# Kernel optimization log

Hardware: AMD Instinct MI355X
Metric: run time of the kernel (lower is better)

Reference implementation:

```python
import jax, jax.numpy as jnp
import numpy as np

B, S, D, H = 2, 2048, 1024, 16
HD = D // H  # head_dim = 64
SCALE = HD ** -0.5


def setup_inputs() -> dict:
    key = jax.random.key(0)
    k1, k2, k3 = jax.random.split(key, 3)
    src = jax.random.normal(k1, (B, S, D), dtype=jnp.float32)
    w_qkv = jax.random.normal(k2, (D, 3 * D), dtype=jnp.float32) * (D ** -0.5)
    b_qkv = jax.random.normal(k3, (3 * D,), dtype=jnp.float32) * 0.02
    return {"src": src, "w_qkv": w_qkv, "b_qkv": b_qkv}


def reference(src, w_qkv, b_qkv):
    # qkv projection: [B,S,3D]
    qkv = src @ w_qkv + b_qkv
    q, k, v = jnp.split(qkv, 3, axis=-1)
    # [B,S,D] -> [B,H,S,HD]
    def heads(x):
        return x.reshape(B, S, H, HD).transpose(0, 2, 1, 3)
    q, k, v = heads(q), heads(k), heads(v)
    # scaled dot-product attention (note: original scales AFTER q@k.T)
    attn = jnp.einsum('bhqd,bhkd->bhqk', q, k) * SCALE
    attn = jax.nn.softmax(attn, axis=-1)
    out = jnp.einsum('bhqk,bhkd->bhqd', attn, v)  # [B,H,S,HD]
    return out.transpose(0, 2, 1, 3).reshape(B, S, D)
```

## Files before the change

kernel.cpp:

```cpp
#include <hip/hip_runtime.h>
#include <hip/hip_bf16.h>

typedef short short8 __attribute__((ext_vector_type(8)));
typedef float f32x4 __attribute__((ext_vector_type(4)));
typedef float f32x16 __attribute__((ext_vector_type(16)));
typedef __hip_bfloat16 bf16;


__device__ __forceinline__ void glds16(const void* g, void* l) {
  __builtin_amdgcn_global_load_lds((const __attribute__((address_space(1))) unsigned int*)g,
                                   (__attribute__((address_space(3))) unsigned int*)l, 16, 0, 0);
}

__device__ __forceinline__ uint pk2(float a, float b) {
  union { bf16 h2[2]; uint u; } pk;
  pk.h2[0] = __float2bfloat16(a);
  pk.h2[1] = __float2bfloat16(b);
  return pk.u;
}

__global__ __launch_bounds__(256) void cvt_src_kernel(const float4* __restrict__ in,
                                                      bf16* __restrict__ out, int n4) {
  int i = blockIdx.x * 256 + threadIdx.x;
  if (i >= n4) return;
  float4 v = in[i];
  union { bf16 h[4]; uint2 u; } pk;
  pk.h[0] = __float2bfloat16(v.x);
  pk.h[1] = __float2bfloat16(v.y);
  pk.h[2] = __float2bfloat16(v.z);
  pk.h[3] = __float2bfloat16(v.w);
  *(uint2*)(out + (size_t)i * 4) = pk.u;
}

__global__ __launch_bounds__(256) void transpose_w_kernel(const float* __restrict__ w,
                                                          bf16* __restrict__ wt) {
  __shared__ float tile[32][33];
  int x0 = blockIdx.x * 32;
  int y0 = blockIdx.y * 32;
  int tx = threadIdx.x & 31, ty = threadIdx.x >> 5;
#pragma unroll
  for (int i = 0; i < 4; i++) {
    int y = ty + i * 8;
    tile[y][tx] = w[(size_t)(y0 + y) * 3072 + x0 + tx];
  }
  __syncthreads();
#pragma unroll
  for (int i = 0; i < 4; i++) {
    int y = ty + i * 8;
    wt[(size_t)(x0 + y) * 1024 + y0 + tx] = __float2bfloat16(tile[tx][y]);
  }
}

__global__ __launch_bounds__(256) void qkv_gemm_kernel(
    const bf16* __restrict__ A, const bf16* __restrict__ Bt,
    const float* __restrict__ bias,
    bf16* __restrict__ q_ws, bf16* __restrict__ k_ws, bf16* __restrict__ vt_ws) {
  __shared__ alignas(16) char AB[32768];
  const int tid = threadIdx.x;
  const int lane = tid & 63, wid = tid >> 6;
  const int lr = lane & 15, lg = lane >> 4;
  const int wm = wid >> 1, wn = wid & 1;
  const int m0 = blockIdx.x * 128, n0 = blockIdx.y * 128;

  const f32x4 z4 = {0.f, 0.f, 0.f, 0.f};
  f32x4 acc[4][4];
#pragma unroll
  for (int m = 0; m < 4; m++)
#pragma unroll
    for (int n = 0; n < 4; n++) acc[m][n] = z4;

  const int srow = lane >> 3;
  const int sseg = (lane & 7) ^ srow;
  const char* Ag = (const char*)A + (size_t)(m0 + wid * 32 + srow) * 2048 + sseg * 16;
  const char* Bg = (const char*)Bt + (size_t)(n0 + wid * 32 + srow) * 2048 + sseg * 16;
  char* Al = AB + wid * 4096;
  char* Bl = AB + 16384 + wid * 4096;
  const int xora = (lr & 7) << 4;

  for (int kt = 0; kt < 16; kt++) {
    __syncthreads();
#pragma unroll
    for (int c = 0; c < 4; c++) {
      glds16(Ag + (size_t)kt * 128 + c * 16384, Al + c * 1024);
      glds16(Bg + (size_t)kt * 128 + c * 16384, Bl + c * 1024);
    }
    asm volatile("s_waitcnt vmcnt(0)" ::: "memory");
    __syncthreads();
#pragma unroll
    for (int g = 0; g < 2; g++) {
      short8 af[4], bfr[4];
#pragma unroll
      for (int m = 0; m < 4; m++)
        af[m] = *(const short8*)(AB + (wm * 64 + m * 16 + lr) * 128 +
                                 ((g * 64 + lg * 16) ^ xora));
#pragma unroll
      for (int n = 0; n < 4; n++)
        bfr[n] = *(const short8*)(AB + 16384 + (wn * 64 + n * 16 + lr) * 128 +
                                  ((g * 64 + lg * 16) ^ xora));
#pragma unroll
      for (int m = 0; m < 4; m++)
#pragma unroll
        for (int n = 0; n < 4; n++)
          acc[m][n] = __builtin_amdgcn_mfma_f32_16x16x32_bf16(af[m], bfr[n], acc[m][n], 0, 0, 0);
    }
  }

  const int which = n0 >> 10;
#pragma unroll
  for (int m = 0; m < 4; m++) {
    int row = m0 + wm * 64 + m * 16 + lg * 4;
    int b = row >> 11;
    int ss0 = row & 2047;
#pragma unroll
    for (int n = 0; n < 4; n++) {
      int col = n0 + wn * 64 + n * 16 + lr;
      int d = col & 1023;
      int h = d >> 6, hd = d & 63;
      size_t bh = (size_t)(b * 16 + h);
      float bv = bias[col];
      if (which == 2) {
        union { bf16 h4[4]; uint2 u; } pk;
#pragma unroll
        for (int r = 0; r < 4; r++) pk.h4[r] = __float2bfloat16(acc[m][n][r] + bv);
        *(uint2*)&vt_ws[(bh * 64 + hd) * 2048 + ss0] = pk.u;
      } else {
        bf16* dst = (which == 0) ? q_ws : k_ws;
#pragma unroll
        for (int r = 0; r < 4; r++)
          dst[(bh * 2048 + (ss0 + r)) * 64 + hd] = __float2bfloat16(acc[m][n][r] + bv);
      }
    }
  }
}

__global__ __launch_bounds__(512) void attn3_kernel(
    const bf16* __restrict__ q_ws, const bf16* __restrict__ k_ws,
    const bf16* __restrict__ vt_ws, float* __restrict__ out) {
  __shared__ alignas(16) char smem[65536];
  const int tid = threadIdx.x;
  const int lane = tid & 63, wid = tid >> 6;
  const int lq = lane & 31, hi = lane >> 5;
  const int hi16 = hi * 16;
  const int xorv = (lq & 7) << 4;
  const float scale_l2e = 0.125f * 1.44269504088896f;

  const int f = blockIdx.x;
  const int bh = (f & 7) * 4 + ((f >> 3) & 3);
  const int qb = f >> 5;
  const int b = bh >> 4, h = bh & 15;
  const int q0 = qb * 256 + wid * 32;

  short8 qf[4];
  {
    const bf16* qrow = q_ws + ((size_t)bh * 2048 + q0 + lq) * 64;
#pragma unroll
    for (int s = 0; s < 4; s++) qf[s] = *(const short8*)(qrow + s * 16 + hi * 8);
  }

  const int l8 = lane >> 3;
  const int segk = (lane & 7) ^ l8;
  const char* kgl = (const char*)k_ws + (size_t)bh * 262144 +
                    (size_t)(wid * 16 + l8) * 128 + segk * 16;
  const int l16 = lane >> 4;
  const int d0v = (wid * 2 + 0) * 4 + l16;
  const int d1v = (wid * 2 + 1) * 4 + l16;
  const char* vg0 = (const char*)vt_ws + (size_t)bh * 262144 + (size_t)d0v * 4096 +
                    (((lane & 15) ^ (d0v & 15)) << 4);
  const char* vg1 = (const char*)vt_ws + (size_t)bh * 262144 + (size_t)d1v * 4096 +
                    (((lane & 15) ^ (d1v & 15)) << 4);

  f32x16 o0a, o0b, o1a, o1b;
#pragma unroll
  for (int r = 0; r < 16; r++) { o0a[r] = 0.f; o0b[r] = 0.f; o1a[r] = 0.f; o1b[r] = 0.f; }
  float m = -1e30f, l = 0.f;

  glds16(kgl, smem + wid * 2048);
  glds16(kgl + 1024, smem + wid * 2048 + 1024);
  glds16(vg0, smem + 32768 + wid * 2048);
  glds16(vg1, smem + 32768 + wid * 2048 + 1024);
  asm volatile("s_waitcnt vmcnt(0)" ::: "memory");
  __builtin_amdgcn_s_barrier();

  for (int kt = 0; kt < 16; ++kt) {
    const int kb_off = (kt & 1) * 16384;
    const int vb_off = 32768 + (kt & 1) * 16384;
    if (kt + 1 < 16) {
      const int nb = ((kt + 1) & 1) * 16384;
      glds16(kgl + (size_t)(kt + 1) * 16384, smem + nb + wid * 2048);
      glds16(kgl + (size_t)(kt + 1) * 16384 + 1024, smem + nb + wid * 2048 + 1024);
      glds16(vg0 + (size_t)(kt + 1) * 256, smem + 32768 + nb + wid * 2048);
      glds16(vg1 + (size_t)(kt + 1) * 256, smem + 32768 + nb + wid * 2048 + 1024);
    }

    f32x16 s0, s1, s2, s3;
#pragma unroll
    for (int r = 0; r < 16; r++) { s0[r] = 0.f; s1[r] = 0.f; s2[r] = 0.f; s3[r] = 0.f; }
#pragma unroll
    for (int st = 0; st < 4; st++) {
      const int doff = (st * 32 + hi16) ^ xorv;
      short8 ka = *(const short8*)(smem + kb_off + lq * 128 + doff);
      short8 kb = *(const short8*)(smem + kb_off + (lq + 32) * 128 + doff);
      short8 kc = *(const short8*)(smem + kb_off + (lq + 64) * 128 + doff);
      short8 kd = *(const short8*)(smem + kb_off + (lq + 96) * 128 + doff);
      __builtin_amdgcn_s_setprio(1);
      s0 = __builtin_amdgcn_mfma_f32_32x32x16_bf16(ka, qf[st], s0, 0, 0, 0);
      s1 = __builtin_amdgcn_mfma_f32_32x32x16_bf16(kb, qf[st], s1, 0, 0, 0);
      s2 = __builtin_amdgcn_mfma_f32_32x32x16_bf16(kc, qf[st], s2, 0, 0, 0);
      s3 = __builtin_amdgcn_mfma_f32_32x32x16_bf16(kd, qf[st], s3, 0, 0, 0);
      __builtin_amdgcn_s_setprio(0);
    }

    float mx[16];
#pragma unroll
    for (int i = 0; i < 16; i++)
      mx[i] = fmaxf(fmaxf(s0[i], s1[i]), fmaxf(s2[i], s3[i]));
#pragma unroll
    for (int i = 0; i < 8; i++) mx[i] = fmaxf(mx[i], mx[i + 8]);
#pragma unroll
    for (int i = 0; i < 4; i++) mx[i] = fmaxf(mx[i], mx[i + 4]);
    float pm = fmaxf(fmaxf(mx[0], mx[1]), fmaxf(mx[2], mx[3]));
    pm = fmaxf(pm, __shfl_xor(pm, 32));
    pm *= scale_l2e;
    if (pm > m + 8.f) {
      float rs = __builtin_amdgcn_exp2f(m - pm);
      m = pm; l *= rs;
#pragma unroll
      for (int r = 0; r < 16; r++) {
        o0a[r] *= rs; o0b[r] *= rs; o1a[r] *= rs; o1b[r] *= rs;
      }
    }
#pragma unroll
    for (int r = 0; r < 16; r++) {
      s0[r] = __builtin_amdgcn_exp2f(__builtin_fmaf(s0[r], scale_l2e, -m));
      s1[r] = __builtin_amdgcn_exp2f(__builtin_fmaf(s1[r], scale_l2e, -m));
      s2[r] = __builtin_amdgcn_exp2f(__builtin_fmaf(s2[r], scale_l2e, -m));
      s3[r] = __builtin_amdgcn_exp2f(__builtin_fmaf(s3[r], scale_l2e, -m));
    }
    {
      float sm[16];
#pragma unroll
      for (int i = 0; i < 16; i++) sm[i] = (s0[i] + s1[i]) + (s2[i] + s3[i]);
#pragma unroll
      for (int i = 0; i < 8; i++) sm[i] += sm[i + 8];
#pragma unroll
      for (int i = 0; i < 4; i++) sm[i] += sm[i + 4];
      float ps = (sm[0] + sm[1]) + (sm[2] + sm[3]);
      ps += __shfl_xor(ps, 32);
      l += ps;
    }

#define PV_KB(S, KB, OA, OB)                                                     \
  {                                                                              \
    uint w0 = pk2(S[0], S[1]), w1 = pk2(S[2], S[3]);                             \
    uint w2 = pk2(S[4], S[5]), w3 = pk2(S[6], S[7]);                             \
    uint w4 = pk2(S[8], S[9]), w5 = pk2(S[10], S[11]);                           \
    uint w6 = pk2(S[12], S[13]), w7 = pk2(S[14], S[15]);                         \
    uint r0 = (uint)__shfl_xor((int)(hi ? w0 : w2), 32);                         \
    uint r1 = (uint)__shfl_xor((int)(hi ? w1 : w3), 32);                         \
    uint r2 = (uint)__shfl_xor((int)(hi ? w4 : w6), 32);                         \
    uint r3 = (uint)__shfl_xor((int)(hi ? w5 : w7), 32);                         \
    union { uint u[4]; short8 s8; } ua, ub;                                      \
    ua.u[0] = hi ? r0 : w0; ua.u[1] = hi ? r1 : w1;                              \
    ua.u[2] = hi ? w2 : r0; ua.u[3] = hi ? w3 : r1;                              \
    ub.u[0] = hi ? r2 : w4; ub.u[1] = hi ? r3 : w5;                              \
    ub.u[2] = hi ? w6 : r2; ub.u[3] = hi ? w7 : r3;                              \
    const int c0 = (((KB) * 4 + hi) ^ (lq & 15)) << 4;                           \
    const int c1 = (((KB) * 4 + 2 + hi) ^ (lq & 15)) << 4;                       \
    short8 va0 = *(const short8*)(smem + vb_off + lq * 256 + c0);                \
    short8 va1 = *(const short8*)(smem + vb_off + (lq + 32) * 256 + c0);         \
    short8 vb0 = *(const short8*)(smem + vb_off + lq * 256 + c1);                \
    short8 vb1 = *(const short8*)(smem + vb_off + (lq + 32) * 256 + c1);         \
    __builtin_amdgcn_s_setprio(1);                                               \
    OA = __builtin_amdgcn_mfma_f32_32x32x16_bf16(va0, ua.s8, OA, 0, 0, 0);       \
    OB = __builtin_amdgcn_mfma_f32_32x32x16_bf16(va1, ua.s8, OB, 0, 0, 0);       \
    OA = __builtin_amdgcn_mfma_f32_32x32x16_bf16(vb0, ub.s8, OA, 0, 0, 0);       \
    OB = __builtin_amdgcn_mfma_f32_32x32x16_bf16(vb1, ub.s8, OB, 0, 0, 0);       \
    __builtin_amdgcn_s_setprio(0);                                               \
  }
    PV_KB(s0, 0, o0a, o1a)
    PV_KB(s1, 1, o0b, o1b)
    PV_KB(s2, 2, o0a, o1a)
    PV_KB(s3, 3, o0b, o1b)
#undef PV_KB

    if (kt < 15) {
      asm volatile("s_waitcnt vmcnt(0)" ::: "memory");
      __builtin_amdgcn_s_barrier();
    }
  }
  __syncthreads();

  f32x16 o0, o1;
#pragma unroll
  for (int r = 0; r < 16; r++) { o0[r] = o0a[r] + o0b[r]; o1[r] = o1a[r] + o1b[r]; }
  float* ep = (float*)(smem) + wid * 1024;
  const float invl = 1.f / l;
  const int eq = lane >> 1, eds = lane & 1;
  float* obase = out + ((size_t)b * 2048 + qb * 256 + wid * 32 + eq) * 1024 +
                 h * 64 + eds * 16;
#pragma unroll
  for (int db = 0; db < 2; db++) {
#pragma unroll
    for (int r = 0; r < 16; r++) {
      int d = (r & 3) + 8 * (r >> 2) + 4 * hi;
      float v = (db ? o1[r] : o0[r]) * invl;
      ep[lq * 32 + ((d + lq) & 31)] = v;
    }
#pragma unroll
    for (int c = 0; c < 4; c++) {
      float4 t;
      t.x = ep[eq * 32 + ((eds * 16 + 4 * c + 0 + eq) & 31)];
      t.y = ep[eq * 32 + ((eds * 16 + 4 * c + 1 + eq) & 31)];
      t.z = ep[eq * 32 + ((eds * 16 + 4 * c + 2 + eq) & 31)];
      t.w = ep[eq * 32 + ((eds * 16 + 4 * c + 3 + eq) & 31)];
      *(float4*)(obase + db * 32 + 4 * c) = t;
    }
  }
}

extern "C" void kernel_launch(void* const* d_in, const int* in_sizes, int n_in,
                              void* d_out, int out_size, void* d_ws, size_t ws_size,
                              hipStream_t stream) {
  (void)in_sizes; (void)n_in; (void)out_size; (void)ws_size;
  const float* src  = (const float*)d_in[0];
  const float* w    = (const float*)d_in[1];
  const float* bias = (const float*)d_in[2];
  float* out = (float*)d_out;

  char* ws = (char*)d_ws;
  bf16* src_bf = (bf16*)ws;
  bf16* wt_bf  = (bf16*)(ws + 8388608);
  bf16* q_ws   = (bf16*)(ws + 8388608 + 6291456);
  bf16* k_ws   = q_ws + 4194304;
  bf16* vt_ws  = k_ws + 4194304;

  cvt_src_kernel<<<4096, 256, 0, stream>>>((const float4*)src, src_bf, 1048576);
  transpose_w_kernel<<<dim3(96, 32), 256, 0, stream>>>(w, wt_bf);
  qkv_gemm_kernel<<<dim3(32, 24), 256, 0, stream>>>(src_bf, wt_bf, bias, q_ws, k_ws, vt_ws);
  attn3_kernel<<<256, 512, 0, stream>>>(q_ws, k_ws, vt_ws, out);
}
```

Baseline: 102.7 us.

## Software-pipeline attention QK^T of next tile with softmax/PV of current; merge prep kernels

The attention kernel is restructured so the QK^T MFMAs for tile T+1 are interleaved with exp and PV work for tile T, using ping-pong score registers. K is prefetched two tiles ahead with partial vmcnt waits. The split o0a/o0b accumulators are collapsed into two, and launch bounds ask for 2 waves per SIMD. Separately, the src conversion and weight transpose kernels are merged into one launch to cut launch overhead. This adds register pressure and more barriers per iteration.

```diff
diff --git a/kernel.cpp b/kernel.cpp
--- a/kernel.cpp
+++ b/kernel.cpp
@@ -19,35 +19,37 @@
   return pk.u;
 }
 
-__global__ __launch_bounds__(256) void cvt_src_kernel(const float4* __restrict__ in,
-                                                      bf16* __restrict__ out, int n4) {
-  int i = blockIdx.x * 256 + threadIdx.x;
-  if (i >= n4) return;
-  float4 v = in[i];
-  union { bf16 h[4]; uint2 u; } pk;
-  pk.h[0] = __float2bfloat16(v.x);
-  pk.h[1] = __float2bfloat16(v.y);
-  pk.h[2] = __float2bfloat16(v.z);
-  pk.h[3] = __float2bfloat16(v.w);
-  *(uint2*)(out + (size_t)i * 4) = pk.u;
-}
-
-__global__ __launch_bounds__(256) void transpose_w_kernel(const float* __restrict__ w,
-                                                          bf16* __restrict__ wt) {
+__global__ __launch_bounds__(256) void prep_kernel(const float4* __restrict__ in,
+                                                   bf16* __restrict__ src_bf,
+                                                   const float* __restrict__ w,
+                                                   bf16* __restrict__ wt) {
   __shared__ float tile[32][33];
-  int x0 = blockIdx.x * 32;
-  int y0 = blockIdx.y * 32;
-  int tx = threadIdx.x & 31, ty = threadIdx.x >> 5;
-#pragma unroll
-  for (int i = 0; i < 4; i++) {
-    int y = ty + i * 8;
-    tile[y][tx] = w[(size_t)(y0 + y) * 3072 + x0 + tx];
-  }
-  __syncthreads();
-#pragma unroll
-  for (int i = 0; i < 4; i++) {
-    int y = ty + i * 8;
-    wt[(size_t)(x0 + y) * 1024 + y0 + tx] = __float2bfloat16(tile[tx][y]);
+  const int bid = blockIdx.x;
+  if (bid < 4096) {
+    int i = bid * 256 + threadIdx.x;
+    float4 v = in[i];
+    union { bf16 h[4]; uint2 u; } pk;
+    pk.h[0] = __float2bfloat16(v.x);
+    pk.h[1] = __float2bfloat16(v.y);
+    pk.h[2] = __float2bfloat16(v.z);
+    pk.h[3] = __float2bfloat16(v.w);
+    *(uint2*)(src_bf + (size_t)i * 4) = pk.u;
+  } else {
+    int id = bid - 4096;
+    int x0 = (id % 96) * 32;
+    int y0 = (id / 96) * 32;
+    int tx = threadIdx.x & 31, ty = threadIdx.x >> 5;
+#pragma unroll
+    for (int i = 0; i < 4; i++) {
+      int y = ty + i * 8;
+      tile[y][tx] = w[(size_t)(y0 + y) * 3072 + x0 + tx];
+    }
+    __syncthreads();
+#pragma unroll
+    for (int i = 0; i < 4; i++) {
+      int y = ty + i * 8;
+      wt[(size_t)(x0 + y) * 1024 + y0 + tx] = __float2bfloat16(tile[tx][y]);
+    }
   }
 }
 
@@ -133,7 +135,121 @@
   }
 }
 
-__global__ __launch_bounds__(512) void attn3_kernel(
+#define PV_KB(S, KB)                                                           \
+  {                                                                            \
+    uint w0 = pk2(S[0], S[1]), w1 = pk2(S[2], S[3]);                           \
+    uint w2 = pk2(S[4], S[5]), w3 = pk2(S[6], S[7]);                           \
+    uint w4 = pk2(S[8], S[9]), w5 = pk2(S[10], S[11]);                         \
+    uint w6 = pk2(S[12], S[13]), w7 = pk2(S[14], S[15]);                       \
+    uint r0 = (uint)__shfl_xor((int)(hi ? w0 : w2), 32);                       \
+    uint r1 = (uint)__shfl_xor((int)(hi ? w1 : w3), 32);                       \
+    uint r2 = (uint)__shfl_xor((int)(hi ? w4 : w6), 32);                       \
+    uint r3 = (uint)__shfl_xor((int)(hi ? w5 : w7), 32);                       \
+    union { uint u[4]; short8 s8; } ua, ub;                                    \
+    ua.u[0] = hi ? r0 : w0; ua.u[1] = hi ? r1 : w1;                            \
+    ua.u[2] = hi ? w2 : r0; ua.u[3] = hi ? w3 : r1;                            \
+    ub.u[0] = hi ? r2 : w4; ub.u[1] = hi ? r3 : w5;                            \
+    ub.u[2] = hi ? w6 : r2; ub.u[3] = hi ? w7 : r3;                            \
+    const int c0 = (((KB) * 4 + hi) ^ (lq & 15)) << 4;                         \
+    const int c1 = (((KB) * 4 + 2 + hi) ^ (lq & 15)) << 4;                     \
+    short8 va0 = *(const short8*)(smem + vbc + lq * 256 + c0);                 \
+    short8 va1 = *(const short8*)(smem + vbc + (lq + 32) * 256 + c0);          \
+    short8 vb0 = *(const short8*)(smem + vbc + lq * 256 + c1);                 \
+    short8 vb1 = *(const short8*)(smem + vbc + (lq + 32) * 256 + c1);          \
+    __builtin_amdgcn_s_setprio(1);                                             \
+    o0 = __builtin_amdgcn_mfma_f32_32x32x16_bf16(va0, ua.s8, o0, 0, 0, 0);     \
+    o1 = __builtin_amdgcn_mfma_f32_32x32x16_bf16(va1, ua.s8, o1, 0, 0, 0);     \
+    o0 = __builtin_amdgcn_mfma_f32_32x32x16_bf16(vb0, ub.s8, o0, 0, 0, 0);     \
+    o1 = __builtin_amdgcn_mfma_f32_32x32x16_bf16(vb1, ub.s8, o1, 0, 0, 0);     \
+    __builtin_amdgcn_s_setprio(0);                                             \
+  }
+
+#define QK_ST(ST, AR, B0, B1, B2, B3, QKF, KBN)                                \
+  {                                                                            \
+    if (QKF) {                                                                 \
+      const int doff = ((ST) * 32 + hi16) ^ xorv;                              \
+      short8 ka = *(const short8*)(smem + (KBN) + lq * 128 + doff);            \
+      short8 kb = *(const short8*)(smem + (KBN) + (lq + 32) * 128 + doff);     \
+      short8 kc = *(const short8*)(smem + (KBN) + (lq + 64) * 128 + doff);     \
+      short8 kd = *(const short8*)(smem + (KBN) + (lq + 96) * 128 + doff);     \
+      __builtin_amdgcn_s_setprio(1);                                           \
+      B0 = __builtin_amdgcn_mfma_f32_32x32x16_bf16(ka, qf[ST], B0, 0, 0, 0);   \
+      B1 = __builtin_amdgcn_mfma_f32_32x32x16_bf16(kb, qf[ST], B1, 0, 0, 0);   \
+      B2 = __builtin_amdgcn_mfma_f32_32x32x16_bf16(kc, qf[ST], B2, 0, 0, 0);   \
+      B3 = __builtin_amdgcn_mfma_f32_32x32x16_bf16(kd, qf[ST], B3, 0, 0, 0);   \
+      __builtin_amdgcn_s_setprio(0);                                           \
+    }                                                                          \
+    _Pragma("unroll")                                                          \
+    for (int r_ = 0; r_ < 16; r_++)                                            \
+      AR[r_] = __builtin_amdgcn_exp2f(__builtin_fmaf(AR[r_], scale_l2e, -m));  \
+  }
+
+#define ATTN_ITER(T, A0, A1, A2, A3, B0, B1, B2, B3, VMC, KF, VF, QKF, EB)     \
+  {                                                                            \
+    if (KF) {                                                                  \
+      glds16(kgl + (size_t)((T) + 2) * 16384,                                  \
+             smem + ((T) & 1) * 16384 + wid * 2048);                           \
+      glds16(kgl + (size_t)((T) + 2) * 16384 + 1024,                           \
+             smem + ((T) & 1) * 16384 + wid * 2048 + 1024);                    \
+    }                                                                          \
+    if (VF) {                                                                  \
+      glds16(vg0 + (size_t)((T) + 1) * 256,                                    \
+             smem + 32768 + (((T) + 1) & 1) * 16384 + wid * 2048);             \
+      glds16(vg1 + (size_t)((T) + 1) * 256,                                    \
+             smem + 32768 + (((T) + 1) & 1) * 16384 + wid * 2048 + 1024);      \
+    }                                                                          \
+    asm volatile("s_waitcnt vmcnt(" #VMC ")" ::: "memory");                    \
+    __builtin_amdgcn_s_barrier();                                              \
+    const int kbn = (((T) + 1) & 1) * 16384;                                   \
+    const int vbc = 32768 + ((T) & 1) * 16384;                                 \
+    if (QKF) {                                                                 \
+      _Pragma("unroll") for (int r_ = 0; r_ < 16; r_++) {                      \
+        B0[r_] = 0.f; B1[r_] = 0.f; B2[r_] = 0.f; B3[r_] = 0.f;                \
+      }                                                                        \
+    }                                                                          \
+    QK_ST(0, A0, B0, B1, B2, B3, QKF, kbn)                                     \
+    QK_ST(1, A1, B0, B1, B2, B3, QKF, kbn)                                     \
+    QK_ST(2, A2, B0, B1, B2, B3, QKF, kbn)                                     \
+    QK_ST(3, A3, B0, B1, B2, B3, QKF, kbn)                                     \
+    {                                                                          \
+      float sm_[16];                                                           \
+      _Pragma("unroll") for (int i = 0; i < 16; i++)                           \
+        sm_[i] = (A0[i] + A1[i]) + (A2[i] + A3[i]);                            \
+      _Pragma("unroll") for (int i = 0; i < 8; i++) sm_[i] += sm_[i + 8];      \
+      _Pragma("unroll") for (int i = 0; i < 4; i++) sm_[i] += sm_[i + 4];      \
+      float ps = (sm_[0] + sm_[1]) + (sm_[2] + sm_[3]);                        \
+      ps += __shfl_xor(ps, 32);                                                \
+      l += ps;                                                                 \
+    }                                                                          \
+    PV_KB(A0, 0)                                                               \
+    PV_KB(A1, 1)                                                               \
+    PV_KB(A2, 2)                                                               \
+    PV_KB(A3, 3)                                                               \
+    if (QKF) {                                                                 \
+      float mx_[16];                                                           \
+      _Pragma("unroll") for (int i = 0; i < 16; i++)                           \
+        mx_[i] = fmaxf(fmaxf(B0[i], B1[i]), fmaxf(B2[i], B3[i]));              \
+      _Pragma("unroll") for (int i = 0; i < 8; i++)                            \
+        mx_[i] = fmaxf(mx_[i], mx_[i + 8]);                                    \
+      _Pragma("unroll") for (int i = 0; i < 4; i++)                            \
+        mx_[i] = fmaxf(mx_[i], mx_[i + 4]);                                    \
+      float pm = fmaxf(fmaxf(mx_[0], mx_[1]), fmaxf(mx_[2], mx_[3]));          \
+      pm = fmaxf(pm, __shfl_xor(pm, 32));                                      \
+      pm *= scale_l2e;                                                         \
+      if (pm > m + 8.f) {                                                      \
+        float rs = __builtin_amdgcn_exp2f(m - pm);                             \
+        m = pm;                                                                \
+        l *= rs;                                                               \
+        _Pragma("unroll") for (int r_ = 0; r_ < 16; r_++) {                    \
+          o0[r_] *= rs;                                                        \
+          o1[r_] *= rs;                                                        \
+        }                                                                      \
+      }                                                                        \
+    }                                                                          \
+    if (EB) __builtin_amdgcn_s_barrier();                                      \
+  }
+
+__global__ __launch_bounds__(512, 2) void attn4_kernel(
     const bf16* __restrict__ q_ws, const bf16* __restrict__ k_ws,
     const bf16* __restrict__ vt_ws, float* __restrict__ out) {
   __shared__ alignas(16) char smem[65536];
@@ -162,137 +278,71 @@
   const char* kgl = (const char*)k_ws + (size_t)bh * 262144 +
                     (size_t)(wid * 16 + l8) * 128 + segk * 16;
   const int l16 = lane >> 4;
-  const int d0v = (wid * 2 + 0) * 4 + l16;
-  const int d1v = (wid * 2 + 1) * 4 + l16;
+  const int d0v = wid * 8 + l16;
+  const int d1v = wid * 8 + 4 + l16;
   const char* vg0 = (const char*)vt_ws + (size_t)bh * 262144 + (size_t)d0v * 4096 +
                     (((lane & 15) ^ (d0v & 15)) << 4);
   const char* vg1 = (const char*)vt_ws + (size_t)bh * 262144 + (size_t)d1v * 4096 +
                     (((lane & 15) ^ (d1v & 15)) << 4);
-
-  f32x16 o0a, o0b, o1a, o1b;
-#pragma unroll
-  for (int r = 0; r < 16; r++) { o0a[r] = 0.f; o0b[r] = 0.f; o1a[r] = 0.f; o1b[r] = 0.f; }
+  char* kl0 = smem + wid * 2048;
+  char* vl0 = smem + 32768 + wid * 2048;
+
+  f32x16 o0, o1, a0, a1, a2, a3, b0, b1, b2, b3;
+#pragma unroll
+  for (int r = 0; r < 16; r++) { o0[r] = 0.f; o1[r] = 0.f; }
   float m = -1e30f, l = 0.f;
 
-  glds16(kgl, smem + wid * 2048);
-  glds16(kgl + 1024, smem + wid * 2048 + 1024);
-  glds16(vg0, smem + 32768 + wid * 2048);
-  glds16(vg1, smem + 32768 + wid * 2048 + 1024);
-  asm volatile("s_waitcnt vmcnt(0)" ::: "memory");
+  glds16(kgl, kl0);
+  glds16(kgl + 1024, kl0 + 1024);
+  glds16(kgl + 16384, kl0 + 16384);
+  glds16(kgl + 16384 + 1024, kl0 + 16384 + 1024);
+  glds16(vg0, vl0);
+  glds16(vg1, vl0 + 1024);
+  asm volatile("s_waitcnt vmcnt(4)" ::: "memory");
   __builtin_amdgcn_s_barrier();
-
-  for (int kt = 0; kt < 16; ++kt) {
-    const int kb_off = (kt & 1) * 16384;
-    const int vb_off = 32768 + (kt & 1) * 16384;
-    if (kt + 1 < 16) {
-      const int nb = ((kt + 1) & 1) * 16384;
-      glds16(kgl + (size_t)(kt + 1) * 16384, smem + nb + wid * 2048);
-      glds16(kgl + (size_t)(kt + 1) * 16384 + 1024, smem + nb + wid * 2048 + 1024);
-      glds16(vg0 + (size_t)(kt + 1) * 256, smem + 32768 + nb + wid * 2048);
-      glds16(vg1 + (size_t)(kt + 1) * 256, smem + 32768 + nb + wid * 2048 + 1024);
-    }
-
-    f32x16 s0, s1, s2, s3;
-#pragma unroll
-    for (int r = 0; r < 16; r++) { s0[r] = 0.f; s1[r] = 0.f; s2[r] = 0.f; s3[r] = 0.f; }
-#pragma unroll
-    for (int st = 0; st < 4; st++) {
-      const int doff = (st * 32 + hi16) ^ xorv;
-      short8 ka = *(const short8*)(smem + kb_off + lq * 128 + doff);
-      short8 kb = *(const short8*)(smem + kb_off + (lq + 32) * 128 + doff);
-      short8 kc = *(const short8*)(smem + kb_off + (lq + 64) * 128 + doff);
-      short8 kd = *(const short8*)(smem + kb_off + (lq + 96) * 128 + doff);
-      __builtin_amdgcn_s_setprio(1);
-      s0 = __builtin_amdgcn_mfma_f32_32x32x16_bf16(ka, qf[st], s0, 0, 0, 0);
-      s1 = __builtin_amdgcn_mfma_f32_32x32x16_bf16(kb, qf[st], s1, 0, 0, 0);
-      s2 = __builtin_amdgcn_mfma_f32_32x32x16_bf16(kc, qf[st], s2, 0, 0, 0);
-      s3 = __builtin_amdgcn_mfma_f32_32x32x16_bf16(kd, qf[st], s3, 0, 0, 0);
-      __builtin_amdgcn_s_setprio(0);
-    }
-
-    float mx[16];
+#pragma unroll
+  for (int r = 0; r < 16; r++) { a0[r] = 0.f; a1[r] = 0.f; a2[r] = 0.f; a3[r] = 0.f; }
+#pragma unroll
+  for (int st = 0; st < 4; st++) {
+    const int doff = (st * 32 + hi16) ^ xorv;
+    short8 ka = *(const short8*)(smem + lq * 128 + doff);
+    short8 kb = *(const short8*)(smem + (lq + 32) * 128 + doff);
+    short8 kc = *(const short8*)(smem + (lq + 64) * 128 + doff);
+    short8 kd = *(const short8*)(smem + (lq + 96) * 128 + doff);
+    __builtin_amdgcn_s_setprio(1);
+    a0 = __builtin_amdgcn_mfma_f32_32x32x16_bf16(ka, qf[st], a0, 0, 0, 0);
+    a1 = __builtin_amdgcn_mfma_f32_32x32x16_bf16(kb, qf[st], a1, 0, 0, 0);
+    a2 = __builtin_amdgcn_mfma_f32_32x32x16_bf16(kc, qf[st], a2, 0, 0, 0);
+    a3 = __builtin_amdgcn_mfma_f32_32x32x16_bf16(kd, qf[st], a3, 0, 0, 0);
+    __builtin_amdgcn_s_setprio(0);
+  }
+  {
+    float mx_[16];
 #pragma unroll
     for (int i = 0; i < 16; i++)
-      mx[i] = fmaxf(fmaxf(s0[i], s1[i]), fmaxf(s2[i], s3[i]));
-#pragma unroll
-    for (int i = 0; i < 8; i++) mx[i] = fmaxf(mx[i], mx[i + 8]);
-#pragma unroll
-    for (int i = 0; i < 4; i++) mx[i] = fmaxf(mx[i], mx[i + 4]);
-    float pm = fmaxf(fmaxf(mx[0], mx[1]), fmaxf(mx[2], mx[3]));
+      mx_[i] = fmaxf(fmaxf(a0[i], a1[i]), fmaxf(a2[i], a3[i]));
+#pragma unroll
+    for (int i = 0; i < 8; i++) mx_[i] = fmaxf(mx_[i], mx_[i + 8]);
+#pragma unroll
+    for (int i = 0; i < 4; i++) mx_[i] = fmaxf(mx_[i], mx_[i + 4]);
+    float pm = fmaxf(fmaxf(mx_[0], mx_[1]), fmaxf(mx_[2], mx_[3]));
     pm = fmaxf(pm, __shfl_xor(pm, 32));
     pm *= scale_l2e;
-    if (pm > m + 8.f) {
-      float rs = __builtin_amdgcn_exp2f(m - pm);
-      m = pm; l *= rs;
-#pragma unroll
-      for (int r = 0; r < 16; r++) {
-        o0a[r] *= rs; o0b[r] *= rs; o1a[r] *= rs; o1b[r] *= rs;
-      }
-    }
-#pragma unroll
-    for (int r = 0; r < 16; r++) {
-      s0[r] = __builtin_amdgcn_exp2f(__builtin_fmaf(s0[r], scale_l2e, -m));
-      s1[r] = __builtin_amdgcn_exp2f(__builtin_fmaf(s1[r], scale_l2e, -m));
-      s2[r] = __builtin_amdgcn_exp2f(__builtin_fmaf(s2[r], scale_l2e, -m));
-      s3[r] = __builtin_amdgcn_exp2f(__builtin_fmaf(s3[r], scale_l2e, -m));
-    }
-    {
-      float sm[16];
-#pragma unroll
-      for (int i = 0; i < 16; i++) sm[i] = (s0[i] + s1[i]) + (s2[i] + s3[i]);
-#pragma unroll
-      for (int i = 0; i < 8; i++) sm[i] += sm[i + 8];
-#pragma unroll
-      for (int i = 0; i < 4; i++) sm[i] += sm[i + 4];
-      float ps = (sm[0] + sm[1]) + (sm[2] + sm[3]);
-      ps += __shfl_xor(ps, 32);
-      l += ps;
-    }
-
-#define PV_KB(S, KB, OA, OB)                                                     \
-  {                                                                              \
-    uint w0 = pk2(S[0], S[1]), w1 = pk2(S[2], S[3]);                             \
-    uint w2 = pk2(S[4], S[5]), w3 = pk2(S[6], S[7]);                             \
-    uint w4 = pk2(S[8], S[9]), w5 = pk2(S[10], S[11]);                           \
-    uint w6 = pk2(S[12], S[13]), w7 = pk2(S[14], S[15]);                         \
-    uint r0 = (uint)__shfl_xor((int)(hi ? w0 : w2), 32);                         \
-    uint r1 = (uint)__shfl_xor((int)(hi ? w1 : w3), 32);                         \
-    uint r2 = (uint)__shfl_xor((int)(hi ? w4 : w6), 32);                         \
-    uint r3 = (uint)__shfl_xor((int)(hi ? w5 : w7), 32);                         \
-    union { uint u[4]; short8 s8; } ua, ub;                                      \
-    ua.u[0] = hi ? r0 : w0; ua.u[1] = hi ? r1 : w1;                              \
-    ua.u[2] = hi ? w2 : r0; ua.u[3] = hi ? w3 : r1;                              \
-    ub.u[0] = hi ? r2 : w4; ub.u[1] = hi ? r3 : w5;                              \
-    ub.u[2] = hi ? w6 : r2; ub.u[3] = hi ? w7 : r3;                              \
-    const int c0 = (((KB) * 4 + hi) ^ (lq & 15)) << 4;                           \
-    const int c1 = (((KB) * 4 + 2 + hi) ^ (lq & 15)) << 4;                       \
-    short8 va0 = *(const short8*)(smem + vb_off + lq * 256 + c0);                \
-    short8 va1 = *(const short8*)(smem + vb_off + (lq + 32) * 256 + c0);         \
-    short8 vb0 = *(const short8*)(smem + vb_off + lq * 256 + c1);                \
-    short8 vb1 = *(const short8*)(smem + vb_off + (lq + 32) * 256 + c1);         \
-    __builtin_amdgcn_s_setprio(1);                                               \
-    OA = __builtin_amdgcn_mfma_f32_32x32x16_bf16(va0, ua.s8, OA, 0, 0, 0);       \
-    OB = __builtin_amdgcn_mfma_f32_32x32x16_bf16(va1, ua.s8, OB, 0, 0, 0);       \
-    OA = __builtin_amdgcn_mfma_f32_32x32x16_bf16(vb0, ub.s8, OA, 0, 0, 0);       \
-    OB = __builtin_amdgcn_mfma_f32_32x32x16_bf16(vb1, ub.s8, OB, 0, 0, 0);       \
-    __builtin_amdgcn_s_setprio(0);                                               \
-  }
-    PV_KB(s0, 0, o0a, o1a)
-    PV_KB(s1, 1, o0b, o1b)
-    PV_KB(s2, 2, o0a, o1a)
-    PV_KB(s3, 3, o0b, o1b)
-#undef PV_KB
-
-    if (kt < 15) {
-      asm volatile("s_waitcnt vmcnt(0)" ::: "memory");
-      __builtin_amdgcn_s_barrier();
-    }
-  }
+    m = pm;
+  }
+  __builtin_amdgcn_s_barrier();
+
+  for (int tt = 0; tt < 7; ++tt) {
+    const int T0 = 2 * tt;
+    const int T1 = 2 * tt + 1;
+    ATTN_ITER(T0, a0, a1, a2, a3, b0, b1, b2, b3, 4, 1, 1, 1, 1)
+    ATTN_ITER(T1, b0, b1, b2, b3, a0, a1, a2, a3, 4, 1, 1, 1, 1)
+  }
+  ATTN_ITER(14, a0, a1, a2, a3, b0, b1, b2, b3, 2, 0, 1, 1, 1)
+  ATTN_ITER(15, b0, b1, b2, b3, a0, a1, a2, a3, 0, 0, 0, 0, 0)
+
   __syncthreads();
 
-  f32x16 o0, o1;
-#pragma unroll
-  for (int r = 0; r < 16; r++) { o0[r] = o0a[r] + o0b[r]; o1[r] = o1a[r] + o1b[r]; }
   float* ep = (float*)(smem) + wid * 1024;
   const float invl = 1.f / l;
   const int eq = lane >> 1, eds = lane & 1;
@@ -334,8 +384,7 @@
   bf16* k_ws   = q_ws + 4194304;
   bf16* vt_ws  = k_ws + 4194304;
 
-  cvt_src_kernel<<<4096, 256, 0, stream>>>((const float4*)src, src_bf, 1048576);
-  transpose_w_kernel<<<dim3(96, 32), 256, 0, stream>>>(w, wt_bf);
+  prep_kernel<<<7168, 256, 0, stream>>>((const float4*)src, src_bf, w, wt_bf);
   qkv_gemm_kernel<<<dim3(32, 24), 256, 0, stream>>>(src_bf, wt_bf, bias, q_ws, k_ws, vt_ws);
-  attn3_kernel<<<256, 512, 0, stream>>>(q_ws, k_ws, vt_ws, out);
-}
+  attn4_kernel<<<256, 512, 0, stream>>>(q_ws, k_ws, vt_ws, out);
+}
```

Result: faster. 100.6 us (-2.1%).

## Merge prep kernels and rewrite QKV GEMM with 256x192 tiles and 4-stage async pipeline

Applied to the files above, without the earlier changes.

Merges the source conversion and weight transpose into one launch to save a kernel launch. Rewrites the QKV GEMM to use 512-thread blocks with 256x192 tiles, giving exactly 256 blocks (one wave on the CUs) mapped per XCD for L2 locality. It also adds a 4-slot LDS ring with direct global-to-LDS prefetch three K-steps ahead, interleaved with MFMA groups and s_setprio. Larger tiles cut operand re-reads and overlap loads with compute, at the cost of more registers and 112KB of LDS per block.

```diff
diff --git a/kernel.cpp b/kernel.cpp
--- a/kernel.cpp
+++ b/kernel.cpp
@@ -19,115 +19,164 @@
   return pk.u;
 }
 
-__global__ __launch_bounds__(256) void cvt_src_kernel(const float4* __restrict__ in,
-                                                      bf16* __restrict__ out, int n4) {
-  int i = blockIdx.x * 256 + threadIdx.x;
-  if (i >= n4) return;
-  float4 v = in[i];
-  union { bf16 h[4]; uint2 u; } pk;
-  pk.h[0] = __float2bfloat16(v.x);
-  pk.h[1] = __float2bfloat16(v.y);
-  pk.h[2] = __float2bfloat16(v.z);
-  pk.h[3] = __float2bfloat16(v.w);
-  *(uint2*)(out + (size_t)i * 4) = pk.u;
-}
-
-__global__ __launch_bounds__(256) void transpose_w_kernel(const float* __restrict__ w,
-                                                          bf16* __restrict__ wt) {
+__global__ __launch_bounds__(256) void prep_kernel(const float4* __restrict__ in,
+                                                   bf16* __restrict__ src_bf,
+                                                   const float* __restrict__ w,
+                                                   bf16* __restrict__ wt) {
   __shared__ float tile[32][33];
-  int x0 = blockIdx.x * 32;
-  int y0 = blockIdx.y * 32;
-  int tx = threadIdx.x & 31, ty = threadIdx.x >> 5;
-#pragma unroll
-  for (int i = 0; i < 4; i++) {
-    int y = ty + i * 8;
-    tile[y][tx] = w[(size_t)(y0 + y) * 3072 + x0 + tx];
-  }
-  __syncthreads();
-#pragma unroll
-  for (int i = 0; i < 4; i++) {
-    int y = ty + i * 8;
-    wt[(size_t)(x0 + y) * 1024 + y0 + tx] = __float2bfloat16(tile[tx][y]);
-  }
-}
-
-__global__ __launch_bounds__(256) void qkv_gemm_kernel(
+  const int bid = blockIdx.x;
+  if (bid < 4096) {
+    int i = bid * 256 + threadIdx.x;
+    float4 v = in[i];
+    union { bf16 h[4]; uint2 u; } pk;
+    pk.h[0] = __float2bfloat16(v.x);
+    pk.h[1] = __float2bfloat16(v.y);
+    pk.h[2] = __float2bfloat16(v.z);
+    pk.h[3] = __float2bfloat16(v.w);
+    *(uint2*)(src_bf + (size_t)i * 4) = pk.u;
+  } else {
+    int id = bid - 4096;
+    int x0 = (id % 96) * 32;
+    int y0 = (id / 96) * 32;
+    int tx = threadIdx.x & 31, ty = threadIdx.x >> 5;
+#pragma unroll
+    for (int i = 0; i < 4; i++) {
+      int y = ty + i * 8;
+      tile[y][tx] = w[(size_t)(y0 + y) * 3072 + x0 + tx];
+    }
+    __syncthreads();
+#pragma unroll
+    for (int i = 0; i < 4; i++) {
+      int y = ty + i * 8;
+      wt[(size_t)(x0 + y) * 1024 + y0 + tx] = __float2bfloat16(tile[tx][y]);
+    }
+  }
+}
+
+__global__ __launch_bounds__(512) void qkv_gemm_kernel(
     const bf16* __restrict__ A, const bf16* __restrict__ Bt,
     const float* __restrict__ bias,
     bf16* __restrict__ q_ws, bf16* __restrict__ k_ws, bf16* __restrict__ vt_ws) {
-  __shared__ alignas(16) char AB[32768];
+  __shared__ alignas(16) char smem[114688];
   const int tid = threadIdx.x;
   const int lane = tid & 63, wid = tid >> 6;
   const int lr = lane & 15, lg = lane >> 4;
-  const int wm = wid >> 1, wn = wid & 1;
-  const int m0 = blockIdx.x * 128, n0 = blockIdx.y * 128;
+  const int wm = wid >> 2, wn = wid & 3;
+
+  const int f = blockIdx.x;
+  const int xcd = f & 7, ii = f >> 3;
+  const int by = xcd * 2 + (ii >> 4);
+  const int bx = ii & 15;
+  const int m0 = bx * 256, n0 = by * 192;
+
+  const int fswz = ((lr & 3) ^ ((lr >> 2) & 3)) << 4;
+
+  const int srow = lane >> 2, sseg0 = lane & 3;
+  const int ar0 = wid * 16 + srow, ar1 = 128 + wid * 16 + srow;
+  const int br0 = wid * 16 + srow, br1 = 128 + wid * 8 + srow;
+  const char* Ag0 = (const char*)A + (size_t)(m0 + ar0) * 2048 +
+                    ((sseg0 ^ (ar0 & 3) ^ ((ar0 >> 2) & 3)) << 4);
+  const char* Ag1 = (const char*)A + (size_t)(m0 + ar1) * 2048 +
+                    ((sseg0 ^ (ar1 & 3) ^ ((ar1 >> 2) & 3)) << 4);
+  const char* Bg0 = (const char*)Bt + (size_t)(n0 + br0) * 2048 +
+                    ((sseg0 ^ (br0 & 3) ^ ((br0 >> 2) & 3)) << 4);
+  const char* Bg1 = (const char*)Bt + (size_t)(n0 + br1) * 2048 +
+                    ((sseg0 ^ (br1 & 3) ^ ((br1 >> 2) & 3)) << 4);
 
   const f32x4 z4 = {0.f, 0.f, 0.f, 0.f};
-  f32x4 acc[4][4];
-#pragma unroll
-  for (int m = 0; m < 4; m++)
-#pragma unroll
-    for (int n = 0; n < 4; n++) acc[m][n] = z4;
-
-  const int srow = lane >> 3;
-  const int sseg = (lane & 7) ^ srow;
-  const char* Ag = (const char*)A + (size_t)(m0 + wid * 32 + srow) * 2048 + sseg * 16;
-  const char* Bg = (const char*)Bt + (size_t)(n0 + wid * 32 + srow) * 2048 + sseg * 16;
-  char* Al = AB + wid * 4096;
-  char* Bl = AB + 16384 + wid * 4096;
-  const int xora = (lr & 7) << 4;
-
-  for (int kt = 0; kt < 16; kt++) {
-    __syncthreads();
-#pragma unroll
-    for (int c = 0; c < 4; c++) {
-      glds16(Ag + (size_t)kt * 128 + c * 16384, Al + c * 1024);
-      glds16(Bg + (size_t)kt * 128 + c * 16384, Bl + c * 1024);
-    }
-    asm volatile("s_waitcnt vmcnt(0)" ::: "memory");
-    __syncthreads();
-#pragma unroll
-    for (int g = 0; g < 2; g++) {
-      short8 af[4], bfr[4];
-#pragma unroll
-      for (int m = 0; m < 4; m++)
-        af[m] = *(const short8*)(AB + (wm * 64 + m * 16 + lr) * 128 +
-                                 ((g * 64 + lg * 16) ^ xora));
-#pragma unroll
-      for (int n = 0; n < 4; n++)
-        bfr[n] = *(const short8*)(AB + 16384 + (wn * 64 + n * 16 + lr) * 128 +
-                                  ((g * 64 + lg * 16) ^ xora));
-#pragma unroll
-      for (int m = 0; m < 4; m++)
-#pragma unroll
-        for (int n = 0; n < 4; n++)
-          acc[m][n] = __builtin_amdgcn_mfma_f32_16x16x32_bf16(af[m], bfr[n], acc[m][n], 0, 0, 0);
-    }
-  }
-
-  const int which = n0 >> 10;
-#pragma unroll
-  for (int m = 0; m < 4; m++) {
-    int row = m0 + wm * 64 + m * 16 + lg * 4;
-    int b = row >> 11;
-    int ss0 = row & 2047;
-#pragma unroll
-    for (int n = 0; n < 4; n++) {
-      int col = n0 + wn * 64 + n * 16 + lr;
-      int d = col & 1023;
-      int h = d >> 6, hd = d & 63;
-      size_t bh = (size_t)(b * 16 + h);
-      float bv = bias[col];
+  f32x4 acc[8][3];
+#pragma unroll
+  for (int mp = 0; mp < 8; mp++)
+#pragma unroll
+    for (int np = 0; np < 3; np++) acc[mp][np] = z4;
+
+#pragma unroll
+  for (int p = 0; p < 3; p++) {
+    const int da = p * 16384, db = 65536 + p * 12288;
+    glds16(Ag0 + (size_t)p * 64, smem + da + wid * 1024);
+    glds16(Ag1 + (size_t)p * 64, smem + da + 8192 + wid * 1024);
+    glds16(Bg0 + (size_t)p * 64, smem + db + wid * 1024);
+    if (lane < 32) glds16(Bg1 + (size_t)p * 64, smem + db + 8192 + wid * 512);
+  }
+  asm volatile("s_waitcnt vmcnt(8)" ::: "memory");
+  __builtin_amdgcn_s_barrier();
+
+  for (int s = 0; s < 32; ++s) {
+    const int slotA = (s & 3) * 16384;
+    const int slotB = 65536 + (s & 3) * 12288;
+    const int da = ((s + 3) & 3) * 16384;
+    const int db = 65536 + ((s + 3) & 3) * 12288;
+
+    short8 bfr[3];
+#pragma unroll
+    for (int np = 0; np < 3; np++) {
+      const int row = wn * 48 + np * 16 + lr;
+      bfr[np] = *(const short8*)(smem + slotB + row * 64 + ((lg << 4) ^ fswz));
+    }
+    short8 af0[4];
+#pragma unroll
+    for (int mp = 0; mp < 4; mp++) {
+      const int row = wm * 128 + mp * 16 + lr;
+      af0[mp] = *(const short8*)(smem + slotA + row * 64 + ((lg << 4) ^ fswz));
+    }
+    if (s <= 28) {
+      glds16(Ag0 + (size_t)(s + 3) * 64, smem + da + wid * 1024);
+      glds16(Ag1 + (size_t)(s + 3) * 64, smem + da + 8192 + wid * 1024);
+    }
+    __builtin_amdgcn_s_setprio(1);
+#pragma unroll
+    for (int mp = 0; mp < 4; mp++)
+#pragma unroll
+      for (int np = 0; np < 3; np++)
+        acc[mp][np] = __builtin_amdgcn_mfma_f32_16x16x32_bf16(af0[mp], bfr[np], acc[mp][np], 0, 0, 0);
+    __builtin_amdgcn_s_setprio(0);
+    short8 af1[4];
+#pragma unroll
+    for (int mp = 0; mp < 4; mp++) {
+      const int row = wm * 128 + (mp + 4) * 16 + lr;
+      af1[mp] = *(const short8*)(smem + slotA + row * 64 + ((lg << 4) ^ fswz));
+    }
+    if (s <= 28) {
+      glds16(Bg0 + (size_t)(s + 3) * 64, smem + db + wid * 1024);
+      if (lane < 32) glds16(Bg1 + (size_t)(s + 3) * 64, smem + db + 8192 + wid * 512);
+    }
+    __builtin_amdgcn_s_setprio(1);
+#pragma unroll
+    for (int mp = 0; mp < 4; mp++)
+#pragma unroll
+      for (int np = 0; np < 3; np++)
+        acc[mp + 4][np] = __builtin_amdgcn_mfma_f32_16x16x32_bf16(af1[mp], bfr[np], acc[mp + 4][np], 0, 0, 0);
+    __builtin_amdgcn_s_setprio(0);
+
+    if (s <= 28)      asm volatile("s_waitcnt vmcnt(8)" ::: "memory");
+    else if (s == 29) asm volatile("s_waitcnt vmcnt(4)" ::: "memory");
+    else if (s == 30) asm volatile("s_waitcnt vmcnt(0)" ::: "memory");
+    if (s < 31) __builtin_amdgcn_s_barrier();
+  }
+
+#pragma unroll
+  for (int np = 0; np < 3; np++) {
+    const int col = n0 + wn * 48 + np * 16 + lr;
+    const int which = col >> 10;
+    const int d = col & 1023;
+    const int h = d >> 6, hd = d & 63;
+    const float bv = bias[col];
+#pragma unroll
+    for (int mp = 0; mp < 8; mp++) {
+      const int row = m0 + wm * 128 + mp * 16 + lg * 4;
+      const int b = row >> 11;
+      const int ss0 = row & 2047;
+      const size_t bh = (size_t)(b * 16 + h);
       if (which == 2) {
         union { bf16 h4[4]; uint2 u; } pk;
 #pragma unroll
-        for (int r = 0; r < 4; r++) pk.h4[r] = __float2bfloat16(acc[m][n][r] + bv);
+        for (int r = 0; r < 4; r++) pk.h4[r] = __float2bfloat16(acc[mp][np][r] + bv);
         *(uint2*)&vt_ws[(bh * 64 + hd) * 2048 + ss0] = pk.u;
       } else {
         bf16* dst = (which == 0) ? q_ws : k_ws;
 #pragma unroll
         for (int r = 0; r < 4; r++)
-          dst[(bh * 2048 + (ss0 + r)) * 64 + hd] = __float2bfloat16(acc[m][n][r] + bv);
+          dst[(bh * 2048 + (ss0 + r)) * 64 + hd] = __float2bfloat16(acc[mp][np][r] + bv);
       }
     }
   }
@@ -334,8 +383,7 @@
   bf16* k_ws   = q_ws + 4194304;
   bf16* vt_ws  = k_ws + 4194304;
 
-  cvt_src_kernel<<<4096, 256, 0, stream>>>((const float4*)src, src_bf, 1048576);
-  transpose_w_kernel<<<dim3(96, 32), 256, 0, stream>>>(w, wt_bf);
-  qkv_gemm_kernel<<<dim3(32, 24), 256, 0, stream>>>(src_bf, wt_bf, bias, q_ws, k_ws, vt_ws);
+  prep_kernel<<<7168, 256, 0, stream>>>((const float4*)src, src_bf, w, wt_bf);
+  qkv_gemm_kernel<<<256, 512, 0, stream>>>(src_bf, wt_bf, bias, q_ws, k_ws, vt_ws);
   attn3_kernel<<<256, 512, 0, stream>>>(q_ws, k_ws, vt_ws, out);
 }
```

Measured after the change: 101.9 us. No clear change (-0.8%).
